# Optimization experiments

Measured on AMD Instinct MI355X. Metric: run time of the kernel, lower is better.

Reference implementation:

```python
import jax, jax.numpy as jnp
import numpy as np

N_NODES = 8192
N_EDGES = 524288
D_IN = 256
D_OUT = 256


def setup_inputs() -> dict:
    key = jax.random.key(0)
    ks = jax.random.split(key, 8)
    h = jax.random.normal(ks[0], (N_NODES, D_IN), dtype=jnp.float32)
    # Xavier-uniform-like scale for weights
    s = (6.0 / (D_IN + D_OUT)) ** 0.5
    W = jax.random.uniform(ks[1], (D_IN, D_OUT), jnp.float32, -s, s)
    Wq = jax.random.uniform(ks[2], (D_IN, D_OUT), jnp.float32, -s, s)
    bq = jnp.zeros((D_OUT,), jnp.float32)
    Wk = jax.random.uniform(ks[3], (D_IN, D_OUT), jnp.float32, -s, s)
    bk = jnp.zeros((D_OUT,), jnp.float32)
    senders = jax.random.randint(ks[4], (N_EDGES,), 0, N_NODES, dtype=jnp.int64 if jax.config.jax_enable_x64 else jnp.int32)
    receivers = jax.random.randint(ks[5], (N_EDGES,), 0, N_NODES, dtype=jnp.int64 if jax.config.jax_enable_x64 else jnp.int32)
    return {"h": h, "W": W, "Wq": Wq, "bq": bq, "Wk": Wk, "bk": bk,
            "senders": senders, "receivers": receivers}


def reference(h, W, Wq, bq, Wk, bk, senders, receivers):
    # Projected node features: (N, D_OUT)
    h_proj = jnp.dot(h, W)
    # Dense attention logits a = q @ k^T: (N, N), as in the original module
    q = jnp.dot(h, Wq) + bq
    k = jnp.dot(h, Wk) + bk
    a = jnp.dot(q, k.T)
    # Gather per-edge messages and attention weights, weight, scatter-add
    messages = h_proj[senders] * a[senders, receivers][:, None]  # (E, D_OUT)
    aggregated = jax.ops.segment_sum(messages, receivers, num_segments=h.shape[0])
    return jax.nn.relu(aggregated)
```

## Files before the change

kernel.cpp:

```cpp
#include <hip/hip_runtime.h>
#include <stdint.h>

typedef unsigned short u16;
typedef unsigned int u32;
typedef short v8s __attribute__((ext_vector_type(8)));
typedef float v4f __attribute__((ext_vector_type(4)));

#define N_NODES 8192
#define N_EDGES 524288
#define DFEAT 256
#define PADC 160
#define NBKT 128
#define NPA  128
#define EPA  (N_EDGES / NPA)
#define EBCAP 4608

static __device__ __forceinline__ float bflo(u32 u) { return __uint_as_float(u << 16); }
static __device__ __forceinline__ float bfhi(u32 u) { return __uint_as_float(u & 0xffff0000u); }
static __device__ __forceinline__ u16 f2bf(float f) {
    u32 u = __float_as_uint(f);
    return (u16)((u + 0x7fffu + ((u >> 16) & 1u)) >> 16);
}

__global__ void prep_small(const float* __restrict__ w0, const float* __restrict__ w1,
                           const float* __restrict__ w2, const float* __restrict__ h,
                           u16* __restrict__ wt, u16* __restrict__ hb,
                           int* __restrict__ bcnt) {
    int b = blockIdx.x;
    if (b < 48) {
        __shared__ u16 t[64][65];
        int region = b >> 4, tile = b & 15;
        int k0 = (tile >> 2) * 64, n0 = (tile & 3) * 64;
        const float* w = (region == 0) ? w0 : ((region == 1) ? w1 : w2);
        int tx = threadIdx.x & 63, ty = threadIdx.x >> 6;
#pragma unroll
        for (int it = 0; it < 16; it++) {
            int row = it * 4 + ty;
            t[row][tx] = f2bf(w[(k0 + row) * 256 + n0 + tx]);
        }
        __syncthreads();
        u16* o = wt + region * 65536;
#pragma unroll
        for (int it = 0; it < 16; it++) {
            int row = it * 4 + ty;
            o[(n0 + row) * 256 + k0 + tx] = t[tx][row];
        }
    } else if (b == 48) {
        if (threadIdx.x < NBKT) bcnt[threadIdx.x] = 0;
    } else {
        int i = ((b - 49) * 256 + threadIdx.x) * 4;
        float4 v = *(const float4*)(h + i);
        uint2 p;
        p.x = (u32)f2bf(v.x) | ((u32)f2bf(v.y) << 16);
        p.y = (u32)f2bf(v.z) | ((u32)f2bf(v.w) << 16);
        *(uint2*)(hb + i) = p;
    }
}

__global__ __launch_bounds__(256) void partA_gemm(
    const u16* __restrict__ hb, const u16* __restrict__ wt,
    const float* __restrict__ bq, const float* __restrict__ bk,
    const int* __restrict__ recv, const int* __restrict__ send,
    u16* __restrict__ hproj, u16* __restrict__ qbuf, u16* __restrict__ kbuf,
    u32* __restrict__ ebuck, int* __restrict__ bcnt) {
    int b = blockIdx.x;
    int tid = threadIdx.x;
    if (b < NPA) {
        __shared__ int hist[NBKT];
        __shared__ int lstart[NBKT + 1];
        __shared__ int cursor[NBKT];
        __shared__ int gpos[NBKT];
        __shared__ u32 sorted[EPA];
        int e0 = b * EPA;
        int r_[16], s_[16];
#pragma unroll
        for (int i = 0; i < 16; i++) {
            int e = e0 + i * 256 + tid;
            r_[i] = recv[e];
            s_[i] = send[e];
        }
        if (tid < NBKT) hist[tid] = 0;
        __syncthreads();
#pragma unroll
        for (int i = 0; i < 16; i++) atomicAdd(&hist[r_[i] >> 6], 1);
        __syncthreads();
        if (tid == 0) {
            int run = 0;
            for (int k = 0; k < NBKT; k++) { lstart[k] = run; run += hist[k]; }
            lstart[NBKT] = run;
        }
        __syncthreads();
        if (tid < NBKT) {
            cursor[tid] = lstart[tid];
            gpos[tid] = atomicAdd(&bcnt[tid], hist[tid]);
        }
        __syncthreads();
#pragma unroll
        for (int i = 0; i < 16; i++) {
            int key = r_[i] >> 6;
            int pos = atomicAdd(&cursor[key], 1);
            sorted[pos] = ((u32)r_[i] << 13) | (u32)s_[i];
        }
        __syncthreads();
        for (int i = tid; i < EPA; i += 256) {
            int lo = 0, hi = NBKT - 1;
#pragma unroll
            for (int it = 0; it < 7; it++) {
                int mid = (lo + hi + 1) >> 1;
                if (lstart[mid] <= i) lo = mid; else hi = mid - 1;
            }
            int k = lo;
            int dst = gpos[k] + (i - lstart[k]);
            if (dst < EBCAP) ebuck[k * EBCAP + dst] = sorted[i];
        }
    } else {
        int g = b - NPA;
        int wave = tid >> 6, lane = tid & 63;
        int lm = lane & 15, lq = lane >> 4;
        int bx = g & 127, by = g >> 7;
        int m0 = bx * 64 + wave * 16;
        int region = by >> 2, n0b = (by & 3) * 64;
        const u16* wtr = wt + region * 65536;

        v4f acc[4];
#pragma unroll
        for (int nt = 0; nt < 4; nt++) acc[nt] = (v4f){0.f, 0.f, 0.f, 0.f};

        const u16* arow = hb + (m0 + lm) * 256 + lq * 8;
#pragma unroll
        for (int k0 = 0; k0 < 256; k0 += 32) {
            v8s a = *(const v8s*)(arow + k0);
#pragma unroll
            for (int nt = 0; nt < 4; nt++) {
                v8s bb = *(const v8s*)(wtr + (n0b + nt * 16 + lm) * 256 + k0 + lq * 8);
                acc[nt] = __builtin_amdgcn_mfma_f32_16x16x32_bf16(a, bb, acc[nt], 0, 0, 0);
            }
        }
        u16* outp = (region == 0) ? hproj : ((region == 1) ? qbuf : kbuf);
        const float* bias = (region == 1) ? bq : ((region == 2) ? bk : nullptr);
#pragma unroll
        for (int nt = 0; nt < 4; nt++) {
            int nn = n0b + nt * 16 + lm;
            float bv = bias ? bias[nn] : 0.f;
#pragma unroll
            for (int i = 0; i < 4; i++) {
                int m = m0 + lq * 4 + i;
                outp[m * 256 + nn] = f2bf(acc[nt][i] + bv);
            }
        }
    }
}

__global__ __launch_bounds__(256) void partB(const u32* __restrict__ ebuck,
                                             const int* __restrict__ bcnt,
                                             u16* __restrict__ es,
                                             int* __restrict__ cnt) {
    __shared__ int off[64];
    __shared__ uint4 imgv[64 * PADC * 2 / 16];
    u16* image = (u16*)imgv;
    int k = blockIdx.x;
    int tid = threadIdx.x;
    if (tid < 64) off[tid] = 0;
    __syncthreads();
    int size = min(bcnt[k], EBCAP);
    const u32* eb = ebuck + k * EBCAP;
    for (int i = tid; i < size; i += 256) {
        u32 v = eb[i];
        int rl = (int)(v >> 13) & 63;
        int s  = (int)(v & 8191u);
        int pos = atomicAdd(&off[rl], 1);
        if (pos < PADC) image[rl * PADC + pos] = (u16)s;
    }
    __syncthreads();
    uint4* dst = (uint4*)(es + k * 64 * PADC);
    for (int i = tid; i < 64 * PADC * 2 / 16; i += 256) dst[i] = imgv[i];
    if (tid < 64) cnt[k * 64 + tid] = off[tid];
}


#define DOT8(Q) (kr0 * bflo((Q).x) + kr1 * bfhi((Q).x)                        \
               + kr2 * bflo((Q).y) + kr3 * bfhi((Q).y)                        \
               + kr4 * bflo((Q).z) + kr5 * bfhi((Q).z)                        \
               + kr6 * bflo((Q).w) + kr7 * bfhi((Q).w))

#define AXPY(P, H) do {                                                       \
    a0 += (P) * bflo((H).x); a1 += (P) * bfhi((H).x);                         \
    a2 += (P) * bflo((H).y); a3 += (P) * bfhi((H).y);                         \
    a4 += (P) * bflo((H).z); a5 += (P) * bfhi((H).z);                         \
    a6 += (P) * bflo((H).w); a7 += (P) * bfhi((H).w);                         \
} while (0)

#define DOT_AGG1(SIDX) do {                                                   \
    int off_ = (int)(SIDX) * 256 + cb;                                        \
    uint4 qv_ = *(const uint4*)(qbuf + off_);                                 \
    uint4 hv_ = *(const uint4*)(hpb + off_);                                  \
    float p_ = DOT8(qv_);                                                     \
    p_ += __shfl_xor(p_, 1, 32);  p_ += __shfl_xor(p_, 2, 32);                \
    p_ += __shfl_xor(p_, 4, 32);  p_ += __shfl_xor(p_, 8, 32);                \
    p_ += __shfl_xor(p_, 16, 32);                                             \
    AXPY(p_, hv_);                                                            \
} while (0)

#define LOAD4(P, SP) do {                                                     \
    int s0_ = (int)((SP).x & 0xffffu), s1_ = (int)((SP).x >> 16);             \
    int s2_ = (int)((SP).y & 0xffffu), s3_ = (int)((SP).y >> 16);             \
    q##P##0 = *(const uint4*)(qbuf + s0_ * 256 + cb);                         \
    h##P##0 = *(const uint4*)(hpb  + s0_ * 256 + cb);                         \
    q##P##1 = *(const uint4*)(qbuf + s1_ * 256 + cb);                         \
    h##P##1 = *(const uint4*)(hpb  + s1_ * 256 + cb);                         \
    q##P##2 = *(const uint4*)(qbuf + s2_ * 256 + cb);                         \
    h##P##2 = *(const uint4*)(hpb  + s2_ * 256 + cb);                         \
    q##P##3 = *(const uint4*)(qbuf + s3_ * 256 + cb);                         \
    h##P##3 = *(const uint4*)(hpb  + s3_ * 256 + cb);                         \
} while (0)

#define COMP4(P) do {                                                         \
    float p0_ = DOT8(q##P##0), p1_ = DOT8(q##P##1);                           \
    float p2_ = DOT8(q##P##2), p3_ = DOT8(q##P##3);                           \
    p0_ += __shfl_xor(p0_, 1, 32);  p1_ += __shfl_xor(p1_, 1, 32);            \
    p2_ += __shfl_xor(p2_, 1, 32);  p3_ += __shfl_xor(p3_, 1, 32);            \
    p0_ += __shfl_xor(p0_, 2, 32);  p1_ += __shfl_xor(p1_, 2, 32);            \
    p2_ += __shfl_xor(p2_, 2, 32);  p3_ += __shfl_xor(p3_, 2, 32);            \
    p0_ += __shfl_xor(p0_, 4, 32);  p1_ += __shfl_xor(p1_, 4, 32);            \
    p2_ += __shfl_xor(p2_, 4, 32);  p3_ += __shfl_xor(p3_, 4, 32);            \
    p0_ += __shfl_xor(p0_, 8, 32);  p1_ += __shfl_xor(p1_, 8, 32);            \
    p2_ += __shfl_xor(p2_, 8, 32);  p3_ += __shfl_xor(p3_, 8, 32);            \
    p0_ += __shfl_xor(p0_, 16, 32); p1_ += __shfl_xor(p1_, 16, 32);           \
    p2_ += __shfl_xor(p2_, 16, 32); p3_ += __shfl_xor(p3_, 16, 32);           \
    AXPY(p0_, h##P##0); AXPY(p1_, h##P##1);                                   \
    AXPY(p2_, h##P##2); AXPY(p3_, h##P##3);                                   \
} while (0)

__global__ __launch_bounds__(256, 4) void edge_fused(
    const u16* __restrict__ qbuf, const u16* __restrict__ kbuf,
    const u16* __restrict__ hpb, const int* __restrict__ cnt,
    const u16* __restrict__ es, float* __restrict__ out) {
    int wave = threadIdx.x >> 6, lane = threadIdx.x & 63;
    int r = blockIdx.x * 4 + wave;
    int lh = lane & 31, half = lane >> 5;
    int cb = lh * 8;
    int n = min(cnt[r], PADC);
    int base = r * PADC;

    uint4 kv = *(const uint4*)(kbuf + r * 256 + cb);
    float kr0 = bflo(kv.x), kr1 = bfhi(kv.x), kr2 = bflo(kv.y), kr3 = bfhi(kv.y),
          kr4 = bflo(kv.z), kr5 = bfhi(kv.z), kr6 = bflo(kv.w), kr7 = bfhi(kv.w);

    float a0 = 0.f, a1 = 0.f, a2 = 0.f, a3 = 0.f,
          a4 = 0.f, a5 = 0.f, a6 = 0.f, a7 = 0.f;

    int NT = n >> 3;
    int m  = n & 7;

    if (NT > 0) {
        uint4 qc0, qc1, qc2, qc3, hc0, hc1, hc2, hc3;
        uint4 qn0, qn1, qn2, qn3, hn0, hn1, hn2, hn3;
        uint2 sa = *(const uint2*)(es + base + half * 4);
        LOAD4(c, sa);
        int t1 = (1 < NT) ? 1 : (NT - 1);
        uint2 sb = *(const uint2*)(es + base + t1 * 8 + half * 4);
        for (int t = 0; t < NT; t += 2) {
            LOAD4(n, sb);
            int t2 = (t + 2 < NT) ? (t + 2) : (NT - 1);
            sa = *(const uint2*)(es + base + t2 * 8 + half * 4);
            COMP4(c);
            if (t + 1 >= NT) break;
            LOAD4(c, sa);
            int t3 = (t + 3 < NT) ? (t + 3) : (NT - 1);
            sb = *(const uint2*)(es + base + t3 * 8 + half * 4);
            COMP4(n);
        }
    }
    if (m > 0) {
        uint2 spT = *(const uint2*)(es + base + NT * 8 + half * 4);
        int mrem = m - half * 4;
        if (mrem > 0) DOT_AGG1(spT.x & 0xffffu);
        if (mrem > 1) DOT_AGG1(spT.x >> 16);
        if (mrem > 2) DOT_AGG1(spT.y & 0xffffu);
        if (mrem > 3) DOT_AGG1(spT.y >> 16);
    }

    a0 += __shfl_xor(a0, 32, 64); a1 += __shfl_xor(a1, 32, 64);
    a2 += __shfl_xor(a2, 32, 64); a3 += __shfl_xor(a3, 32, 64);
    a4 += __shfl_xor(a4, 32, 64); a5 += __shfl_xor(a5, 32, 64);
    a6 += __shfl_xor(a6, 32, 64); a7 += __shfl_xor(a7, 32, 64);

    if (half == 0) {
        float4 o0, o1;
        o0.x = fmaxf(a0, 0.f); o0.y = fmaxf(a1, 0.f);
        o0.z = fmaxf(a2, 0.f); o0.w = fmaxf(a3, 0.f);
        o1.x = fmaxf(a4, 0.f); o1.y = fmaxf(a5, 0.f);
        o1.z = fmaxf(a6, 0.f); o1.w = fmaxf(a7, 0.f);
        float* op = out + r * 256 + cb;
        *(float4*)op = o0;
        *(float4*)(op + 4) = o1;
    }
}

extern "C" void kernel_launch(void* const* d_in, const int* in_sizes, int n_in,
                              void* d_out, int out_size, void* d_ws, size_t ws_size,
                              hipStream_t stream) {
    const float* h  = (const float*)d_in[0];
    const float* W  = (const float*)d_in[1];
    const float* Wq = (const float*)d_in[2];
    const float* bq = (const float*)d_in[3];
    const float* Wk = (const float*)d_in[4];
    const float* bk = (const float*)d_in[5];
    const int* senders   = (const int*)d_in[6];
    const int* receivers = (const int*)d_in[7];
    float* out = (float*)d_out;

    char* ws = (char*)d_ws;
    u16* wt    = (u16*)ws;
    u16* hb    = (u16*)(ws + 393216);
    u16* hproj = hb + N_NODES * DFEAT;
    u16* qbuf  = hproj + N_NODES * DFEAT;
    u16* kbuf  = qbuf + N_NODES * DFEAT;
    int* cnt   = (int*)(kbuf + N_NODES * DFEAT);
    u16* es    = (u16*)(cnt + N_NODES);
    u32* ebuck = (u32*)(es + N_NODES * PADC);
    int* bcnt  = (int*)(ebuck + NBKT * EBCAP);

    prep_small<<<2097, 256, 0, stream>>>(W, Wq, Wk, h, wt, hb, bcnt);
    partA_gemm<<<NPA + 1536, 256, 0, stream>>>(hb, wt, bq, bk, receivers, senders,
                                               hproj, qbuf, kbuf, ebuck, bcnt);
    partB<<<NBKT, 256, 0, stream>>>(ebuck, bcnt, es, cnt);
    edge_fused<<<N_NODES / 4, 256, 0, stream>>>(qbuf, kbuf, hproj, cnt, es, out);
}
```

Measured before the change: 161.3 us.

## Fuse per-receiver edge bucketing into edge kernel and drop partB launch

Removes the separate partB kernel that turned bucketed edges into per-receiver sender lists. Each edge_fused block now rescans its 64-receiver bucket and builds sender lists for its 4 receivers in shared memory, so the es/cnt global round trip and one launch go away. The cost is that each bucket is read 16 times, once per sub-block. It also gets the bucket key from the sorted value instead of a binary search, and adds sched_barriers to the software-pipelined load and compute loop.

```diff
diff --git a/kernel.cpp b/kernel.cpp
--- a/kernel.cpp
+++ b/kernel.cpp
@@ -103,15 +103,10 @@
         }
         __syncthreads();
         for (int i = tid; i < EPA; i += 256) {
-            int lo = 0, hi = NBKT - 1;
-#pragma unroll
-            for (int it = 0; it < 7; it++) {
-                int mid = (lo + hi + 1) >> 1;
-                if (lstart[mid] <= i) lo = mid; else hi = mid - 1;
-            }
-            int k = lo;
+            u32 v = sorted[i];
+            int k = (int)(v >> 19);
             int dst = gpos[k] + (i - lstart[k]);
-            if (dst < EBCAP) ebuck[k * EBCAP + dst] = sorted[i];
+            if (dst < EBCAP) ebuck[k * EBCAP + dst] = v;
         }
     } else {
         int g = b - NPA;
@@ -149,32 +144,6 @@
             }
         }
     }
-}
-
-__global__ __launch_bounds__(256) void partB(const u32* __restrict__ ebuck,
-                                             const int* __restrict__ bcnt,
-                                             u16* __restrict__ es,
-                                             int* __restrict__ cnt) {
-    __shared__ int off[64];
-    __shared__ uint4 imgv[64 * PADC * 2 / 16];
-    u16* image = (u16*)imgv;
-    int k = blockIdx.x;
-    int tid = threadIdx.x;
-    if (tid < 64) off[tid] = 0;
-    __syncthreads();
-    int size = min(bcnt[k], EBCAP);
-    const u32* eb = ebuck + k * EBCAP;
-    for (int i = tid; i < size; i += 256) {
-        u32 v = eb[i];
-        int rl = (int)(v >> 13) & 63;
-        int s  = (int)(v & 8191u);
-        int pos = atomicAdd(&off[rl], 1);
-        if (pos < PADC) image[rl * PADC + pos] = (u16)s;
-    }
-    __syncthreads();
-    uint4* dst = (uint4*)(es + k * 64 * PADC);
-    for (int i = tid; i < 64 * PADC * 2 / 16; i += 256) dst[i] = imgv[i];
-    if (tid < 64) cnt[k * 64 + tid] = off[tid];
 }
 
 
@@ -233,14 +202,35 @@
 
 __global__ __launch_bounds__(256, 4) void edge_fused(
     const u16* __restrict__ qbuf, const u16* __restrict__ kbuf,
-    const u16* __restrict__ hpb, const int* __restrict__ cnt,
-    const u16* __restrict__ es, float* __restrict__ out) {
-    int wave = threadIdx.x >> 6, lane = threadIdx.x & 63;
-    int r = blockIdx.x * 4 + wave;
+    const u16* __restrict__ hpb, const u32* __restrict__ ebuck,
+    const int* __restrict__ bcnt, float* __restrict__ out) {
+    __shared__ int off[4];
+    __shared__ alignas(16) u16 image[4][PADC];
+    int g = blockIdx.x;
+    int tid = threadIdx.x;
+    int wave = tid >> 6, lane = tid & 63;
+    int k = g >> 4, sub = g & 15;
+
+    if (tid < 4) off[tid] = 0;
+    __syncthreads();
+    int size = min(bcnt[k], EBCAP);
+    const u32* eb = ebuck + k * EBCAP;
+    for (int i = tid; i < size; i += 256) {
+        u32 v = eb[i];
+        int rl = (int)((v >> 13) & 63u);
+        if ((rl >> 2) == sub) {
+            int w = rl & 3;
+            int pos = atomicAdd(&off[w], 1);
+            if (pos < PADC) image[w][pos] = (u16)(v & 8191u);
+        }
+    }
+    __syncthreads();
+
+    int r = g * 4 + wave;
     int lh = lane & 31, half = lane >> 5;
     int cb = lh * 8;
-    int n = min(cnt[r], PADC);
-    int base = r * PADC;
+    int n = min(off[wave], PADC);
+    const u16* sbase = image[wave];
 
     uint4 kv = *(const uint4*)(kbuf + r * 256 + cb);
     float kr0 = bflo(kv.x), kr1 = bfhi(kv.x), kr2 = bflo(kv.y), kr3 = bfhi(kv.y),
@@ -255,24 +245,24 @@
     if (NT > 0) {
         uint4 qc0, qc1, qc2, qc3, hc0, hc1, hc2, hc3;
         uint4 qn0, qn1, qn2, qn3, hn0, hn1, hn2, hn3;
-        uint2 sa = *(const uint2*)(es + base + half * 4);
+        uint2 sa = *(const uint2*)(sbase + half * 4);
         LOAD4(c, sa);
-        int t1 = (1 < NT) ? 1 : (NT - 1);
-        uint2 sb = *(const uint2*)(es + base + t1 * 8 + half * 4);
         for (int t = 0; t < NT; t += 2) {
+            int t1 = (t + 1 < NT) ? (t + 1) : (NT - 1);
+            uint2 sb = *(const uint2*)(sbase + t1 * 8 + half * 4);
             LOAD4(n, sb);
-            int t2 = (t + 2 < NT) ? (t + 2) : (NT - 1);
-            sa = *(const uint2*)(es + base + t2 * 8 + half * 4);
+            __builtin_amdgcn_sched_barrier(0);
             COMP4(c);
             if (t + 1 >= NT) break;
+            int t2 = (t + 2 < NT) ? (t + 2) : (NT - 1);
+            sa = *(const uint2*)(sbase + t2 * 8 + half * 4);
             LOAD4(c, sa);
-            int t3 = (t + 3 < NT) ? (t + 3) : (NT - 1);
-            sb = *(const uint2*)(es + base + t3 * 8 + half * 4);
+            __builtin_amdgcn_sched_barrier(0);
             COMP4(n);
         }
     }
     if (m > 0) {
-        uint2 spT = *(const uint2*)(es + base + NT * 8 + half * 4);
+        uint2 spT = *(const uint2*)(sbase + NT * 8 + half * 4);
         int mrem = m - half * 4;
         if (mrem > 0) DOT_AGG1(spT.x & 0xffffu);
         if (mrem > 1) DOT_AGG1(spT.x >> 16);
@@ -316,14 +306,11 @@
     u16* hproj = hb + N_NODES * DFEAT;
     u16* qbuf  = hproj + N_NODES * DFEAT;
     u16* kbuf  = qbuf + N_NODES * DFEAT;
-    int* cnt   = (int*)(kbuf + N_NODES * DFEAT);
-    u16* es    = (u16*)(cnt + N_NODES);
-    u32* ebuck = (u32*)(es + N_NODES * PADC);
+    u32* ebuck = (u32*)(kbuf + N_NODES * DFEAT);
     int* bcnt  = (int*)(ebuck + NBKT * EBCAP);
 
     prep_small<<<2097, 256, 0, stream>>>(W, Wq, Wk, h, wt, hb, bcnt);
     partA_gemm<<<NPA + 1536, 256, 0, stream>>>(hb, wt, bq, bk, receivers, senders,
                                                hproj, qbuf, kbuf, ebuck, bcnt);
-    partB<<<NBKT, 256, 0, stream>>>(ebuck, bcnt, es, cnt);
-    edge_fused<<<N_NODES / 4, 256, 0, stream>>>(qbuf, kbuf, hproj, cnt, es, out);
-}
+    edge_fused<<<N_NODES / 4, 256, 0, stream>>>(qbuf, kbuf, hproj, ebuck, bcnt, out);
+}
```

Measured after the change: 162.0 us. Within noise of the previous version (+0.4%).

## Rebalance stage fusion, interleave q/hproj rows, split edge lists across two waves

Applied to the files above, without the earlier changes.

The edge bucketing pass moves into the prep kernel, and the per-receiver image build moves into the GEMM kernel, which removes one launch. Zeroing of bcnt becomes a memset. The bucket index is now read from the packed key instead of a binary search. q and hproj are stored interleaved per node (512-element stride), so one sender's gathers hit adjacent memory. The edge kernel now uses two waves per receiver that each handle half of the edge tiles and combine their partial sums through shared memory, raising parallelism at the cost of a block-wide sync and a larger block size.

```diff
diff --git a/kernel.cpp b/kernel.cpp
--- a/kernel.cpp
+++ b/kernel.cpp
@@ -14,6 +14,7 @@
 #define NPA  128
 #define EPA  (N_EDGES / NPA)
 #define EBCAP 4608
+#define QHS 512
 
 static __device__ __forceinline__ float bflo(u32 u) { return __uint_as_float(u << 16); }
 static __device__ __forceinline__ float bfhi(u32 u) { return __uint_as_float(u & 0xffff0000u); }
@@ -22,17 +23,19 @@
     return (u16)((u + 0x7fffu + ((u >> 16) & 1u)) >> 16);
 }
 
-__global__ void prep_small(const float* __restrict__ w0, const float* __restrict__ w1,
-                           const float* __restrict__ w2, const float* __restrict__ h,
-                           u16* __restrict__ wt, u16* __restrict__ hb,
-                           int* __restrict__ bcnt) {
+__global__ void prep_mix(const float* __restrict__ w0, const float* __restrict__ w1,
+                         const float* __restrict__ w2, const float* __restrict__ h,
+                         const int* __restrict__ recv, const int* __restrict__ send,
+                         u16* __restrict__ wt, u16* __restrict__ hb,
+                         u32* __restrict__ ebuck, int* __restrict__ bcnt) {
     int b = blockIdx.x;
+    int tid = threadIdx.x;
     if (b < 48) {
         __shared__ u16 t[64][65];
         int region = b >> 4, tile = b & 15;
         int k0 = (tile >> 2) * 64, n0 = (tile & 3) * 64;
         const float* w = (region == 0) ? w0 : ((region == 1) ? w1 : w2);
-        int tx = threadIdx.x & 63, ty = threadIdx.x >> 6;
+        int tx = tid & 63, ty = tid >> 6;
 #pragma unroll
         for (int it = 0; it < 16; it++) {
             int row = it * 4 + ty;
@@ -45,10 +48,51 @@
             int row = it * 4 + ty;
             o[(n0 + row) * 256 + k0 + tx] = t[tx][row];
         }
-    } else if (b == 48) {
-        if (threadIdx.x < NBKT) bcnt[threadIdx.x] = 0;
+    } else if (b < 48 + NPA) {
+        __shared__ int hist[NBKT];
+        __shared__ int lstart[NBKT + 1];
+        __shared__ int cursor[NBKT];
+        __shared__ int gpos[NBKT];
+        __shared__ u32 sorted[EPA];
+        int e0 = (b - 48) * EPA;
+        int r_[16], s_[16];
+#pragma unroll
+        for (int i = 0; i < 16; i++) {
+            int e = e0 + i * 256 + tid;
+            r_[i] = recv[e];
+            s_[i] = send[e];
+        }
+        if (tid < NBKT) hist[tid] = 0;
+        __syncthreads();
+#pragma unroll
+        for (int i = 0; i < 16; i++) atomicAdd(&hist[r_[i] >> 6], 1);
+        __syncthreads();
+        if (tid == 0) {
+            int run = 0;
+            for (int k = 0; k < NBKT; k++) { lstart[k] = run; run += hist[k]; }
+            lstart[NBKT] = run;
+        }
+        __syncthreads();
+        if (tid < NBKT) {
+            cursor[tid] = lstart[tid];
+            gpos[tid] = atomicAdd(&bcnt[tid], hist[tid]);
+        }
+        __syncthreads();
+#pragma unroll
+        for (int i = 0; i < 16; i++) {
+            int key = r_[i] >> 6;
+            int pos = atomicAdd(&cursor[key], 1);
+            sorted[pos] = ((u32)r_[i] << 13) | (u32)s_[i];
+        }
+        __syncthreads();
+        for (int i = tid; i < EPA; i += 256) {
+            u32 v = sorted[i];
+            int k = (int)(v >> 19);
+            int dst = gpos[k] + (i - lstart[k]);
+            if (dst < EBCAP) ebuck[k * EBCAP + dst] = v;
+        }
     } else {
-        int i = ((b - 49) * 256 + threadIdx.x) * 4;
+        int i = ((b - 48 - NPA) * 256 + tid) * 4;
         float4 v = *(const float4*)(h + i);
         uint2 p;
         p.x = (u32)f2bf(v.x) | ((u32)f2bf(v.y) << 16);
@@ -57,64 +101,36 @@
     }
 }
 
-__global__ __launch_bounds__(256) void partA_gemm(
+__global__ __launch_bounds__(256) void gemm_partB(
     const u16* __restrict__ hb, const u16* __restrict__ wt,
     const float* __restrict__ bq, const float* __restrict__ bk,
-    const int* __restrict__ recv, const int* __restrict__ send,
-    u16* __restrict__ hproj, u16* __restrict__ qbuf, u16* __restrict__ kbuf,
-    u32* __restrict__ ebuck, int* __restrict__ bcnt) {
+    const u32* __restrict__ ebuck, const int* __restrict__ bcnt,
+    u16* __restrict__ qh, u16* __restrict__ kbuf,
+    u16* __restrict__ es, int* __restrict__ cnt) {
     int b = blockIdx.x;
     int tid = threadIdx.x;
-    if (b < NPA) {
-        __shared__ int hist[NBKT];
-        __shared__ int lstart[NBKT + 1];
-        __shared__ int cursor[NBKT];
-        __shared__ int gpos[NBKT];
-        __shared__ u32 sorted[EPA];
-        int e0 = b * EPA;
-        int r_[16], s_[16];
-#pragma unroll
-        for (int i = 0; i < 16; i++) {
-            int e = e0 + i * 256 + tid;
-            r_[i] = recv[e];
-            s_[i] = send[e];
-        }
-        if (tid < NBKT) hist[tid] = 0;
-        __syncthreads();
-#pragma unroll
-        for (int i = 0; i < 16; i++) atomicAdd(&hist[r_[i] >> 6], 1);
-        __syncthreads();
-        if (tid == 0) {
-            int run = 0;
-            for (int k = 0; k < NBKT; k++) { lstart[k] = run; run += hist[k]; }
-            lstart[NBKT] = run;
-        }
-        __syncthreads();
-        if (tid < NBKT) {
-            cursor[tid] = lstart[tid];
-            gpos[tid] = atomicAdd(&bcnt[tid], hist[tid]);
-        }
-        __syncthreads();
-#pragma unroll
-        for (int i = 0; i < 16; i++) {
-            int key = r_[i] >> 6;
-            int pos = atomicAdd(&cursor[key], 1);
-            sorted[pos] = ((u32)r_[i] << 13) | (u32)s_[i];
-        }
-        __syncthreads();
-        for (int i = tid; i < EPA; i += 256) {
-            int lo = 0, hi = NBKT - 1;
-#pragma unroll
-            for (int it = 0; it < 7; it++) {
-                int mid = (lo + hi + 1) >> 1;
-                if (lstart[mid] <= i) lo = mid; else hi = mid - 1;
-            }
-            int k = lo;
-            int dst = gpos[k] + (i - lstart[k]);
-            if (dst < EBCAP) ebuck[k * EBCAP + dst] = sorted[i];
-        }
+    if (b < NBKT) {
+        __shared__ int off[64];
+        __shared__ uint4 imgv[64 * PADC * 2 / 16];
+        u16* image = (u16*)imgv;
+        int k = b;
+        if (tid < 64) off[tid] = 0;
+        __syncthreads();
+        int size = min(bcnt[k], EBCAP);
+        const u32* eb = ebuck + k * EBCAP;
+        for (int i = tid; i < size; i += 256) {
+            u32 v = eb[i];
+            int rl = (int)(v >> 13) & 63;
+            int s  = (int)(v & 8191u);
+            int pos = atomicAdd(&off[rl], 1);
+            if (pos < PADC) image[rl * PADC + pos] = (u16)s;
+        }
+        __syncthreads();
+        uint4* dst = (uint4*)(es + k * 64 * PADC);
+        for (int i = tid; i < 64 * PADC * 2 / 16; i += 256) dst[i] = imgv[i];
+        if (tid < 64) cnt[k * 64 + tid] = off[tid];
     } else {
-        int g = b - NPA;
+        int g = b - NBKT;
         int wave = tid >> 6, lane = tid & 63;
         int lm = lane & 15, lq = lane >> 4;
         int bx = g & 127, by = g >> 7;
@@ -136,7 +152,8 @@
                 acc[nt] = __builtin_amdgcn_mfma_f32_16x16x32_bf16(a, bb, acc[nt], 0, 0, 0);
             }
         }
-        u16* outp = (region == 0) ? hproj : ((region == 1) ? qbuf : kbuf);
+        u16* outp = (region == 0) ? (qh + 256) : ((region == 1) ? qh : kbuf);
+        int stride = (region == 2) ? 256 : QHS;
         const float* bias = (region == 1) ? bq : ((region == 2) ? bk : nullptr);
 #pragma unroll
         for (int nt = 0; nt < 4; nt++) {
@@ -145,36 +162,10 @@
 #pragma unroll
             for (int i = 0; i < 4; i++) {
                 int m = m0 + lq * 4 + i;
-                outp[m * 256 + nn] = f2bf(acc[nt][i] + bv);
+                outp[m * stride + nn] = f2bf(acc[nt][i] + bv);
             }
         }
     }
-}
-
-__global__ __launch_bounds__(256) void partB(const u32* __restrict__ ebuck,
-                                             const int* __restrict__ bcnt,
-                                             u16* __restrict__ es,
-                                             int* __restrict__ cnt) {
-    __shared__ int off[64];
-    __shared__ uint4 imgv[64 * PADC * 2 / 16];
-    u16* image = (u16*)imgv;
-    int k = blockIdx.x;
-    int tid = threadIdx.x;
-    if (tid < 64) off[tid] = 0;
-    __syncthreads();
-    int size = min(bcnt[k], EBCAP);
-    const u32* eb = ebuck + k * EBCAP;
-    for (int i = tid; i < size; i += 256) {
-        u32 v = eb[i];
-        int rl = (int)(v >> 13) & 63;
-        int s  = (int)(v & 8191u);
-        int pos = atomicAdd(&off[rl], 1);
-        if (pos < PADC) image[rl * PADC + pos] = (u16)s;
-    }
-    __syncthreads();
-    uint4* dst = (uint4*)(es + k * 64 * PADC);
-    for (int i = tid; i < 64 * PADC * 2 / 16; i += 256) dst[i] = imgv[i];
-    if (tid < 64) cnt[k * 64 + tid] = off[tid];
 }
 
 
@@ -191,9 +182,9 @@
 } while (0)
 
 #define DOT_AGG1(SIDX) do {                                                   \
-    int off_ = (int)(SIDX) * 256 + cb;                                        \
-    uint4 qv_ = *(const uint4*)(qbuf + off_);                                 \
-    uint4 hv_ = *(const uint4*)(hpb + off_);                                  \
+    int off_ = (int)(SIDX) * QHS + cb;                                        \
+    uint4 qv_ = *(const uint4*)(qh + off_);                                   \
+    uint4 hv_ = *(const uint4*)(qh + off_ + 256);                             \
     float p_ = DOT8(qv_);                                                     \
     p_ += __shfl_xor(p_, 1, 32);  p_ += __shfl_xor(p_, 2, 32);                \
     p_ += __shfl_xor(p_, 4, 32);  p_ += __shfl_xor(p_, 8, 32);                \
@@ -204,14 +195,16 @@
 #define LOAD4(P, SP) do {                                                     \
     int s0_ = (int)((SP).x & 0xffffu), s1_ = (int)((SP).x >> 16);             \
     int s2_ = (int)((SP).y & 0xffffu), s3_ = (int)((SP).y >> 16);             \
-    q##P##0 = *(const uint4*)(qbuf + s0_ * 256 + cb);                         \
-    h##P##0 = *(const uint4*)(hpb  + s0_ * 256 + cb);                         \
-    q##P##1 = *(const uint4*)(qbuf + s1_ * 256 + cb);                         \
-    h##P##1 = *(const uint4*)(hpb  + s1_ * 256 + cb);                         \
-    q##P##2 = *(const uint4*)(qbuf + s2_ * 256 + cb);                         \
-    h##P##2 = *(const uint4*)(hpb  + s2_ * 256 + cb);                         \
-    q##P##3 = *(const uint4*)(qbuf + s3_ * 256 + cb);                         \
-    h##P##3 = *(const uint4*)(hpb  + s3_ * 256 + cb);                         \
+    int o0_ = s0_ * QHS + cb, o1_ = s1_ * QHS + cb;                           \
+    int o2_ = s2_ * QHS + cb, o3_ = s3_ * QHS + cb;                           \
+    q##P##0 = *(const uint4*)(qh + o0_);                                      \
+    h##P##0 = *(const uint4*)(qh + o0_ + 256);                                \
+    q##P##1 = *(const uint4*)(qh + o1_);                                      \
+    h##P##1 = *(const uint4*)(qh + o1_ + 256);                                \
+    q##P##2 = *(const uint4*)(qh + o2_);                                      \
+    h##P##2 = *(const uint4*)(qh + o2_ + 256);                                \
+    q##P##3 = *(const uint4*)(qh + o3_);                                      \
+    h##P##3 = *(const uint4*)(qh + o3_ + 256);                                \
 } while (0)
 
 #define COMP4(P) do {                                                         \
@@ -231,12 +224,15 @@
     AXPY(p2_, h##P##2); AXPY(p3_, h##P##3);                                   \
 } while (0)
 
-__global__ __launch_bounds__(256, 4) void edge_fused(
-    const u16* __restrict__ qbuf, const u16* __restrict__ kbuf,
-    const u16* __restrict__ hpb, const int* __restrict__ cnt,
-    const u16* __restrict__ es, float* __restrict__ out) {
-    int wave = threadIdx.x >> 6, lane = threadIdx.x & 63;
-    int r = blockIdx.x * 4 + wave;
+__global__ __launch_bounds__(512, 4) void edge_fused(
+    const u16* __restrict__ qh, const u16* __restrict__ kbuf,
+    const int* __restrict__ cnt, const u16* __restrict__ es,
+    float* __restrict__ out) {
+    __shared__ float lacc[4][256];
+    int tid = threadIdx.x;
+    int wave = tid >> 6, lane = tid & 63;
+    int rw = wave >> 1, part = wave & 1;
+    int r = blockIdx.x * 4 + rw;
     int lh = lane & 31, half = lane >> 5;
     int cb = lh * 8;
     int n = min(cnt[r], PADC);
@@ -251,27 +247,28 @@
 
     int NT = n >> 3;
     int m  = n & 7;
-
-    if (NT > 0) {
+    int NTa = (NT + 1) >> 1;
+    int tBeg = part ? NTa : 0;
+    int tEnd = part ? NT  : NTa;
+
+    if (tBeg < tEnd) {
         uint4 qc0, qc1, qc2, qc3, hc0, hc1, hc2, hc3;
         uint4 qn0, qn1, qn2, qn3, hn0, hn1, hn2, hn3;
-        uint2 sa = *(const uint2*)(es + base + half * 4);
+        uint2 sa = *(const uint2*)(es + base + tBeg * 8 + half * 4);
         LOAD4(c, sa);
-        int t1 = (1 < NT) ? 1 : (NT - 1);
-        uint2 sb = *(const uint2*)(es + base + t1 * 8 + half * 4);
-        for (int t = 0; t < NT; t += 2) {
+        for (int t = tBeg; t < tEnd; t += 2) {
+            int t1 = (t + 1 < tEnd) ? (t + 1) : (tEnd - 1);
+            uint2 sb = *(const uint2*)(es + base + t1 * 8 + half * 4);
             LOAD4(n, sb);
-            int t2 = (t + 2 < NT) ? (t + 2) : (NT - 1);
+            COMP4(c);
+            if (t + 1 >= tEnd) break;
+            int t2 = (t + 2 < tEnd) ? (t + 2) : (tEnd - 1);
             sa = *(const uint2*)(es + base + t2 * 8 + half * 4);
-            COMP4(c);
-            if (t + 1 >= NT) break;
             LOAD4(c, sa);
-            int t3 = (t + 3 < NT) ? (t + 3) : (NT - 1);
-            sb = *(const uint2*)(es + base + t3 * 8 + half * 4);
             COMP4(n);
         }
     }
-    if (m > 0) {
+    if (part == 1 && m > 0) {
         uint2 spT = *(const uint2*)(es + base + NT * 8 + half * 4);
         int mrem = m - half * 4;
         if (mrem > 0) DOT_AGG1(spT.x & 0xffffu);
@@ -285,12 +282,19 @@
     a4 += __shfl_xor(a4, 32, 64); a5 += __shfl_xor(a5, 32, 64);
     a6 += __shfl_xor(a6, 32, 64); a7 += __shfl_xor(a7, 32, 64);
 
-    if (half == 0) {
+    if (part == 1 && half == 0) {
+        float* lp = &lacc[rw][cb];
+        lp[0] = a0; lp[1] = a1; lp[2] = a2; lp[3] = a3;
+        lp[4] = a4; lp[5] = a5; lp[6] = a6; lp[7] = a7;
+    }
+    __syncthreads();
+    if (part == 0 && half == 0) {
+        const float* lp = &lacc[rw][cb];
         float4 o0, o1;
-        o0.x = fmaxf(a0, 0.f); o0.y = fmaxf(a1, 0.f);
-        o0.z = fmaxf(a2, 0.f); o0.w = fmaxf(a3, 0.f);
-        o1.x = fmaxf(a4, 0.f); o1.y = fmaxf(a5, 0.f);
-        o1.z = fmaxf(a6, 0.f); o1.w = fmaxf(a7, 0.f);
+        o0.x = fmaxf(a0 + lp[0], 0.f); o0.y = fmaxf(a1 + lp[1], 0.f);
+        o0.z = fmaxf(a2 + lp[2], 0.f); o0.w = fmaxf(a3 + lp[3], 0.f);
+        o1.x = fmaxf(a4 + lp[4], 0.f); o1.y = fmaxf(a5 + lp[5], 0.f);
+        o1.z = fmaxf(a6 + lp[6], 0.f); o1.w = fmaxf(a7 + lp[7], 0.f);
         float* op = out + r * 256 + cb;
         *(float4*)op = o0;
         *(float4*)(op + 4) = o1;
@@ -313,17 +317,17 @@
     char* ws = (char*)d_ws;
     u16* wt    = (u16*)ws;
     u16* hb    = (u16*)(ws + 393216);
-    u16* hproj = hb + N_NODES * DFEAT;
-    u16* qbuf  = hproj + N_NODES * DFEAT;
-    u16* kbuf  = qbuf + N_NODES * DFEAT;
-    int* cnt   = (int*)(kbuf + N_NODES * DFEAT);
-    u16* es    = (u16*)(cnt + N_NODES);
-    u32* ebuck = (u32*)(es + N_NODES * PADC);
+    u16* qh    = hb + N_NODES * DFEAT;
+    u16* kbuf  = qh + N_NODES * QHS;
+    u16* es    = kbuf + N_NODES * DFEAT;
+    int* cnt   = (int*)(es + N_NODES * PADC);
+    u32* ebuck = (u32*)(cnt + N_NODES);
     int* bcnt  = (int*)(ebuck + NBKT * EBCAP);
 
-    prep_small<<<2097, 256, 0, stream>>>(W, Wq, Wk, h, wt, hb, bcnt);
-    partA_gemm<<<NPA + 1536, 256, 0, stream>>>(hb, wt, bq, bk, receivers, senders,
-                                               hproj, qbuf, kbuf, ebuck, bcnt);
-    partB<<<NBKT, 256, 0, stream>>>(ebuck, bcnt, es, cnt);
-    edge_fused<<<N_NODES / 4, 256, 0, stream>>>(qbuf, kbuf, hproj, cnt, es, out);
-}
+    hipMemsetAsync(bcnt, 0, NBKT * sizeof(int), stream);
+    prep_mix<<<48 + NPA + 2048, 256, 0, stream>>>(W, Wq, Wk, h, receivers, senders,
+                                                  wt, hb, ebuck, bcnt);
+    gemm_partB<<<NBKT + 1536, 256, 0, stream>>>(hb, wt, bq, bk, ebuck, bcnt,
+                                                qh, kbuf, es, cnt);
+    edge_fused<<<N_NODES / 4, 512, 0, stream>>>(qh, kbuf, cnt, es, out);
+}
```

Result: slower. 168.9 us (+4.7%).

## Use one-wave blocks for edge kernel, guard prefetches, drop bucket binary search

Applied to the files above, without the earlier changes.

The edge aggregation kernel now launches one 64-thread block per receiver node instead of four waves per 256-thread block. Each block's runtime then follows only its own node's edge count, and faster blocks retire without waiting on slower waves. The prefetch pipeline is rewritten as a STAGE macro that skips out-of-range loads rather than clamping indices to redundant reloads. In partA the 7-step binary search that finds each sorted entry's bucket is replaced by reading the bucket key from the packed value's high bits. Costs are more blocks to schedule and a changed occupancy hint.

```diff
diff --git a/kernel.cpp b/kernel.cpp
--- a/kernel.cpp
+++ b/kernel.cpp
@@ -103,15 +103,10 @@
         }
         __syncthreads();
         for (int i = tid; i < EPA; i += 256) {
-            int lo = 0, hi = NBKT - 1;
-#pragma unroll
-            for (int it = 0; it < 7; it++) {
-                int mid = (lo + hi + 1) >> 1;
-                if (lstart[mid] <= i) lo = mid; else hi = mid - 1;
-            }
-            int k = lo;
+            u32 v = sorted[i];
+            int k = (int)(v >> 19);
             int dst = gpos[k] + (i - lstart[k]);
-            if (dst < EBCAP) ebuck[k * EBCAP + dst] = sorted[i];
+            if (dst < EBCAP) ebuck[k * EBCAP + dst] = v;
         }
     } else {
         int g = b - NPA;
@@ -231,12 +226,21 @@
     AXPY(p2_, h##P##2); AXPY(p3_, h##P##3);                                   \
 } while (0)
 
-__global__ __launch_bounds__(256, 4) void edge_fused(
+#define STAGE(CUR, NXT, TC) do {                                              \
+    if ((TC) + 1 < NT) {                                                      \
+        LOAD4(NXT, spn);                                                      \
+        if ((TC) + 2 < NT)                                                    \
+            spn = *(const uint2*)(es + base + ((TC) + 2) * 8 + half * 4);     \
+    }                                                                         \
+    COMP4(CUR);                                                               \
+} while (0)
+
+__global__ __launch_bounds__(64, 8) void edge_fused(
     const u16* __restrict__ qbuf, const u16* __restrict__ kbuf,
     const u16* __restrict__ hpb, const int* __restrict__ cnt,
     const u16* __restrict__ es, float* __restrict__ out) {
-    int wave = threadIdx.x >> 6, lane = threadIdx.x & 63;
-    int r = blockIdx.x * 4 + wave;
+    int lane = threadIdx.x & 63;
+    int r = blockIdx.x;
     int lh = lane & 31, half = lane >> 5;
     int cb = lh * 8;
     int n = min(cnt[r], PADC);
@@ -255,20 +259,13 @@
     if (NT > 0) {
         uint4 qc0, qc1, qc2, qc3, hc0, hc1, hc2, hc3;
         uint4 qn0, qn1, qn2, qn3, hn0, hn1, hn2, hn3;
-        uint2 sa = *(const uint2*)(es + base + half * 4);
-        LOAD4(c, sa);
-        int t1 = (1 < NT) ? 1 : (NT - 1);
-        uint2 sb = *(const uint2*)(es + base + t1 * 8 + half * 4);
+        uint2 spc = *(const uint2*)(es + base + half * 4);
+        LOAD4(c, spc);
+        uint2 spn = spc;
+        if (NT > 1) spn = *(const uint2*)(es + base + 8 + half * 4);
         for (int t = 0; t < NT; t += 2) {
-            LOAD4(n, sb);
-            int t2 = (t + 2 < NT) ? (t + 2) : (NT - 1);
-            sa = *(const uint2*)(es + base + t2 * 8 + half * 4);
-            COMP4(c);
-            if (t + 1 >= NT) break;
-            LOAD4(c, sa);
-            int t3 = (t + 3 < NT) ? (t + 3) : (NT - 1);
-            sb = *(const uint2*)(es + base + t3 * 8 + half * 4);
-            COMP4(n);
+            STAGE(c, n, t);
+            if (t + 1 < NT) STAGE(n, c, t + 1);
         }
     }
     if (m > 0) {
@@ -325,5 +322,5 @@
     partA_gemm<<<NPA + 1536, 256, 0, stream>>>(hb, wt, bq, bk, receivers, senders,
                                                hproj, qbuf, kbuf, ebuck, bcnt);
     partB<<<NBKT, 256, 0, stream>>>(ebuck, bcnt, es, cnt);
-    edge_fused<<<N_NODES / 4, 256, 0, stream>>>(qbuf, kbuf, hproj, cnt, es, out);
-}
+    edge_fused<<<N_NODES, 64, 0, stream>>>(qbuf, kbuf, hproj, cnt, es, out);
+}
```

After: 325.1 us. 2.02x slower.
